# Optimization experiments

Measured on AMD Instinct MI355X. Metric: run time of the kernel, lower is better.

The kernel has to match this reference:

```python
import jax, jax.numpy as jnp
import numpy as np
import math

N, T, D = 1024, 4096, 20


def setup_inputs() -> dict:
    key = jax.random.key(0)
    k1, k2, k3, k4, k5 = jax.random.split(key, 5)
    evidence_vector = jax.random.normal(k1, (T, D), jnp.float32)
    # valid (strictly positive) prior and row-stochastic, all-positive transitions
    prior_probs = jax.nn.softmax(jax.random.normal(k2, (N,), jnp.float32))
    transition_probs = jax.nn.softmax(jax.random.normal(k3, (N, N), jnp.float32), axis=1)
    means = jax.random.normal(k4, (N, D), jnp.float32)
    stds = jax.random.uniform(k5, (N, D), jnp.float32, minval=0.5, maxval=1.5)
    emission_paras = jnp.stack([means, stds], axis=-1)  # [N, D, 2]
    return {"evidence_vector": evidence_vector, "prior_probs": prior_probs,
            "transition_probs": transition_probs, "emission_paras": emission_paras}


def _emission_logp(evidence, emission_paras):
    # Faithful to the source: p = (2*pi*std)**(-0.5) * exp(-(x-mean)^2/(2*std^2))
    mean = emission_paras[..., 0]  # [N, D]
    std = emission_paras[..., 1]   # [N, D]
    p = (2.0 * math.pi * std) ** (-0.5) * jnp.exp(
        -(evidence[:, None, :] - mean) ** 2 / (2.0 * std ** 2))  # [T, N, D]
    logp = jnp.log(p)
    # step 0 uses raw log; steps >=1 pass through nan_to_num(nan=0, inf kept)
    logp0 = jnp.sum(logp[0], axis=1)  # [N]
    logp_rest = jnp.sum(jnp.nan_to_num(logp[1:], nan=0.0, posinf=jnp.inf, neginf=-jnp.inf), axis=2)  # [T-1, N]
    return logp0, logp_rest


def _viterbi_nl(evidence, prior, trans, emission_paras):
    logp0, logp_rest = _emission_logp(evidence, emission_paras)
    log_trans = jnp.log(trans)  # all positive transitions -> finite
    col0 = jnp.log(prior) + logp0  # [N]

    state_ids = jnp.arange(N)

    def step(prev_col, logp_t):
        # scores[k, j] = nl[k, i-1] + log trans[k, j]; nl[j,i] = max_k scores + logp
        scores = prev_col[:, None] + log_trans          # [N, N]
        best = jnp.max(scores, axis=0)                  # [N]
        # j == 0 branch of the source: prev_state = j, no max over k
        new0 = prev_col[0] + log_trans[0, 0]
        new_col = jnp.where(state_ids == 0, new0, best) + logp_t
        return new_col, new_col

    _, cols = jax.lax.scan(step, col0, logp_rest)       # [T-1, N]
    nl = jnp.concatenate([col0[None, :], cols], axis=0).T  # [N, T]
    return nl, log_trans


def reference(evidence_vector, prior_probs, transition_probs, emission_paras):
    nl, log_trans = _viterbi_nl(evidence_vector, prior_probs, transition_probs, emission_paras)
    last = jnp.argmax(nl[:, -1]).astype(jnp.int32)

    def bt_step(front, i):
        # argmax_j nl[j, i] + log trans[j, front]; strict '>' ascending -> first max
        best = jnp.argmax(nl[:, i] + log_trans[:, front]).astype(jnp.int32)
        return best, best

    _, rev = jax.lax.scan(bt_step, last, jnp.arange(T - 2, -1, -1))
    # source appends the final argmax twice, then prepends states for i = T-2..0
    sequence = jnp.concatenate([rev[::-1], jnp.array([last, last], dtype=jnp.int32)])
    return sequence  # [T + 1] int32
```

## Files before the change

kernel.cpp:

```cpp
#include <hip/hip_runtime.h>
#include <math.h>

#define NSTATES 1024
#define TT      4096
#define DD      20

#define FW_BLOCKS  64
#define FW_THREADS 256
#define JPB  16
#define NSEG 16
#define KSEG 64

#define SENT 0x7FC00000u

#define OFF_LAT   ((size_t)0)
#define OFF_COLS  ((size_t)20 << 20)
#define OFF_PTR   ((size_t)36 << 20)

typedef unsigned int u32;

__global__ void k_init(uint4* __restrict__ cols4) {
    int id = blockIdx.x * 256 + threadIdx.x;
    cols4[id] = make_uint4(SENT, SENT, SENT, SENT);
}

__global__ void k_logtrans(const float* __restrict__ tr, float* __restrict__ lat) {
    int id = blockIdx.x * 256 + threadIdx.x;
    int k = id >> 10, j = id & 1023;
    lat[(size_t)j * NSTATES + k] = logf(tr[id]);
}

__global__ __launch_bounds__(FW_THREADS, 1) void k_forward(
    const float* __restrict__ lat, const float* __restrict__ ev,
    const float* __restrict__ epar, const float* __restrict__ prior,
    float* __restrict__ cols, unsigned short* __restrict__ bptr)
{
    __shared__ __align__(16) float prevs[NSEG * 68];
    __shared__ float          smaxw[4][JPB];
    __shared__ unsigned short sidxw[4][JPB];
    __shared__ float          elp[2][JPB][DD];
    const int tid  = threadIdx.x;
    const int seg  = tid >> 4;
    const int jj   = tid & (JPB - 1);
    const int wav  = tid >> 6;
    const int j0   = blockIdx.x * JPB;
    const int j    = j0 + jj;
    const float lat00 = lat[0];

    const int jj0e = tid / DD, d0e = tid % DD;
    const float m0 = epar[((size_t)(j0 + jj0e) * DD + d0e) * 2 + 0];
    const float s0 = epar[((size_t)(j0 + jj0e) * DD + d0e) * 2 + 1];
    const float coef0 = 1.0f / sqrtf(6.2831853071795864769f * s0);
    const float den0  = 2.0f * (s0 * s0);
    const bool  has1  = (tid + 256) < JPB * DD;
    const int   it1   = tid + 256;
    const int jj1e = has1 ? it1 / DD : 0, d1e = has1 ? it1 % DD : 0;
    const float m1 = has1 ? epar[((size_t)(j0 + jj1e) * DD + d1e) * 2 + 0] : 0.0f;
    const float s1 = has1 ? epar[((size_t)(j0 + jj1e) * DD + d1e) * 2 + 1] : 1.0f;
    const float coef1 = 1.0f / sqrtf(6.2831853071795864769f * s1);
    const float den1  = 2.0f * (s1 * s1);

    auto emis = [&](int t, int buf) {
        float x0  = ev[(size_t)t * DD + d0e];
        float df0 = x0 - m0;
        float num0 = df0 * df0;
        float p0  = coef0 * expf(-num0 / den0);
        elp[buf][jj0e][d0e] = logf(p0);
        if (has1) {
            float x1  = ev[(size_t)t * DD + d1e];
            float df1 = x1 - m1;
            float num1 = df1 * df1;
            float p1  = coef1 * expf(-num1 / den1);
            elp[buf][jj1e][d1e] = logf(p1);
        }
    };

    float4 latr[16];
    {
        const float* lrow = lat + (size_t)j * NSTATES + seg * KSEG;
        #pragma unroll
        for (int u = 0; u < 16; ++u) latr[u] = *(const float4*)(lrow + u * 4);
    }

    float* dstp = &prevs[(tid >> 4) * 68 + (tid & 15) * 4];
    const float* rowp = &prevs[seg * 68];

    emis(0, 0);
    __syncthreads();
    if (tid < JPB) {
        float acc = 0.0f;
        #pragma unroll
        for (int d = 0; d < DD; ++d) acc += elp[0][tid][d];
        float c0 = logf(prior[j0 + tid]) + acc;
        __hip_atomic_store((u32*)cols + (j0 + tid), __float_as_uint(c0),
                           __ATOMIC_RELAXED, __HIP_MEMORY_SCOPE_AGENT);
    }
    __syncthreads();
    emis(1, 1);
    __syncthreads();
    float esum_reg = 0.0f;
    if (tid < JPB) {
        #pragma unroll
        for (int d = 0; d < DD; ++d) esum_reg += elp[1][tid][d];
    }

    for (int t = 1; t < TT; ++t) {
        const u32* p = (const u32*)(cols + (size_t)(t - 1) * NSTATES) + tid * 4;
        u32 w0, w1, w2, w3;
        for (;;) {
            w0 = __hip_atomic_load(p + 0, __ATOMIC_RELAXED, __HIP_MEMORY_SCOPE_AGENT);
            w1 = __hip_atomic_load(p + 1, __ATOMIC_RELAXED, __HIP_MEMORY_SCOPE_AGENT);
            w2 = __hip_atomic_load(p + 2, __ATOMIC_RELAXED, __HIP_MEMORY_SCOPE_AGENT);
            w3 = __hip_atomic_load(p + 3, __ATOMIC_RELAXED, __HIP_MEMORY_SCOPE_AGENT);
            if (w0 != SENT && w1 != SENT && w2 != SENT && w3 != SENT) break;
            __builtin_amdgcn_s_sleep(1);
        }
        {
            float4 v;
            v.x = __uint_as_float(w0);
            v.y = __uint_as_float(w1);
            v.z = __uint_as_float(w2);
            v.w = __uint_as_float(w3);
            *(float4*)dstp = v;
        }
        __syncthreads();

        float best = -__builtin_inff();
        int bidx = seg * KSEG;
        #pragma unroll
        for (int u = 0; u < 16; ++u) {
            float4 q  = *(const float4*)(rowp + u * 4);
            float4 wv = latr[u];
            int k0 = seg * KSEG + u * 4;
            float v0 = q.x + wv.x;
            float v1 = q.y + wv.y;
            float v2 = q.z + wv.z;
            float v3 = q.w + wv.w;
            if (v0 > best) { best = v0; bidx = k0;     }
            if (v1 > best) { best = v1; bidx = k0 + 1; }
            if (v2 > best) { best = v2; bidx = k0 + 2; }
            if (v3 > best) { best = v3; bidx = k0 + 3; }
        }

        {
            float ov = __shfl_xor(best, 16);
            int   oi = __shfl_xor(bidx, 16);
            if (ov > best || (ov == best && oi < bidx)) { best = ov; bidx = oi; }
            ov = __shfl_xor(best, 32);
            oi = __shfl_xor(bidx, 32);
            if (ov > best || (ov == best && oi < bidx)) { best = ov; bidx = oi; }
        }
        if ((tid & 63) < JPB) {
            smaxw[wav][jj] = best;
            sidxw[wav][jj] = (unsigned short)bidx;
        }
        __syncthreads();

        if (tid < JPB) {
            float m = smaxw[0][tid];
            int  mi = sidxw[0][tid];
            #pragma unroll
            for (int ww = 1; ww < 4; ++ww) {
                float v = smaxw[ww][tid];
                if (v > m) { m = v; mi = sidxw[ww][tid]; }
            }
            int jw = j0 + tid;
            float val = (jw == 0) ? (prevs[0] + lat00) : m;
            float out = val + esum_reg;
            __hip_atomic_store((u32*)(cols + (size_t)t * NSTATES) + jw,
                               __float_as_uint(out), __ATOMIC_RELAXED,
                               __HIP_MEMORY_SCOPE_AGENT);
            bptr[(size_t)t * NSTATES + jw] = (unsigned short)mi;
        }

        if (t + 1 < TT) {
            emis(t + 1, (t + 1) & 1);
            __syncthreads();
            if (tid < JPB) {
                float acc = 0.0f;
                #pragma unroll
                for (int d = 0; d < DD; ++d) acc += elp[(t + 1) & 1][tid][d];
                esum_reg = acc;
            }
        }
    }
}

#define BTC 16
__global__ void k_backtrace(const float* __restrict__ lastcol,
                            const unsigned short* __restrict__ bptr,
                            int* __restrict__ seq)
{
    __shared__ unsigned short ring[2][BTC][NSTATES];
    __shared__ int s_front;
    const int tid = threadIdx.x;

    if (tid < 64) {
        float best = -__builtin_inff();
        int bi = 0;
        for (int n2 = tid; n2 < NSTATES; n2 += 64) {
            float v = lastcol[n2];
            if (v > best) { best = v; bi = n2; }
        }
        #pragma unroll
        for (int off = 32; off > 0; off >>= 1) {
            float ov = __shfl_xor(best, off);
            int   oi = __shfl_xor(bi, off);
            if (ov > best || (ov == best && oi < bi)) { best = ov; bi = oi; }
        }
        if (tid == 0) { seq[TT] = bi; seq[TT - 1] = bi; s_front = bi; }
    }
    __syncthreads();

    auto stage = [&](int c, int buf, int t0, int stride) {
        int rhi = TT - 1 - c * BTC;
        int rlo = rhi - (BTC - 1); if (rlo < 1) rlo = 1;
        int n4 = (rhi - rlo + 1) * 128;
        uint4* dst = (uint4*)&ring[buf][0][0];
        for (int idx = t0; idx < n4; idx += stride) {
            int ro = idx >> 7, wo = idx & 127;
            dst[idx] = ((const uint4*)(bptr + (size_t)(rhi - ro) * NSTATES))[wo];
        }
    };
    const int nc = (TT - 1 + BTC - 1) / BTC;
    stage(0, 0, tid, 256);
    __syncthreads();
    for (int c = 0; c < nc; ++c) {
        int buf = c & 1;
        if (tid != 0) {
            if (c + 1 < nc) stage(c + 1, buf ^ 1, tid - 1, 255);
        } else {
            int rhi = TT - 1 - c * BTC;
            int rlo = rhi - (BTC - 1); if (rlo < 1) rlo = 1;
            int front = s_front;
            for (int r = rhi; r >= rlo; --r) {
                front = (int)ring[buf][rhi - r][front];
                seq[r - 1] = front;
            }
            s_front = front;
        }
        __syncthreads();
    }
}

extern "C" void kernel_launch(void* const* d_in, const int* in_sizes, int n_in,
                              void* d_out, int out_size, void* d_ws, size_t ws_size,
                              hipStream_t stream) {
    const float* ev    = (const float*)d_in[0];
    const float* prior = (const float*)d_in[1];
    const float* tr    = (const float*)d_in[2];
    const float* epar  = (const float*)d_in[3];
    int* seq = (int*)d_out;
    char* ws = (char*)d_ws;
    float* lat  = (float*)(ws + OFF_LAT);
    float* cols = (float*)(ws + OFF_COLS);
    unsigned short* bptr = (unsigned short*)(ws + OFF_PTR);

    k_init<<<4096, 256, 0, stream>>>((uint4*)cols);
    k_logtrans<<<4096, 256, 0, stream>>>(tr, lat);
    k_forward<<<FW_BLOCKS, FW_THREADS, 0, stream>>>(lat, ev, epar, prior, cols, bptr);
    k_backtrace<<<1, 256, 0, stream>>>(cols + (size_t)(TT - 1) * NSTATES, bptr, seq);
}
```

Measured before the change: 9.682 ms.

## Fuse sentinel init and log-transition setup into forward kernel with grid barrier

Removes the separate init and log-transition kernels. Each forward block now fills its own slice of the column buffer with sentinels and computes its log-transition registers directly from the transition matrix, reading it with a strided transposed access. A global atomic counter barrier makes sure every block's sentinel writes are visible before the wavefront loop starts. It also enlarges the backtrace chunk. The ready counter sits at the start of the bptr region, which could clash with bptr writes at t=0 if row 0 is written, and the strided uncoalesced reads of the transition matrix add latency at kernel start.

```diff
diff --git a/kernel.cpp b/kernel.cpp
--- a/kernel.cpp
+++ b/kernel.cpp
@@ -13,27 +13,18 @@
 
 #define SENT 0x7FC00000u
 
-#define OFF_LAT   ((size_t)0)
 #define OFF_COLS  ((size_t)20 << 20)
 #define OFF_PTR   ((size_t)36 << 20)
 
 typedef unsigned int u32;
 
-__global__ void k_init(uint4* __restrict__ cols4) {
-    int id = blockIdx.x * 256 + threadIdx.x;
-    cols4[id] = make_uint4(SENT, SENT, SENT, SENT);
-}
-
-__global__ void k_logtrans(const float* __restrict__ tr, float* __restrict__ lat) {
-    int id = blockIdx.x * 256 + threadIdx.x;
-    int k = id >> 10, j = id & 1023;
-    lat[(size_t)j * NSTATES + k] = logf(tr[id]);
-}
+#define ALD(p) __hip_atomic_load((p), __ATOMIC_RELAXED, __HIP_MEMORY_SCOPE_AGENT)
 
 __global__ __launch_bounds__(FW_THREADS, 1) void k_forward(
-    const float* __restrict__ lat, const float* __restrict__ ev,
+    const float* __restrict__ tr, const float* __restrict__ ev,
     const float* __restrict__ epar, const float* __restrict__ prior,
-    float* __restrict__ cols, unsigned short* __restrict__ bptr)
+    float* __restrict__ cols, unsigned short* __restrict__ bptr,
+    u32* __restrict__ ready)
 {
     __shared__ __align__(16) float prevs[NSEG * 68];
     __shared__ float          smaxw[4][JPB];
@@ -45,7 +36,25 @@
     const int wav  = tid >> 6;
     const int j0   = blockIdx.x * JPB;
     const int j    = j0 + jj;
-    const float lat00 = lat[0];
+
+    {
+        uint4* mine = (uint4*)cols + (size_t)blockIdx.x * (NSTATES * TT / 4 / FW_BLOCKS);
+        const uint4 sv = make_uint4(SENT, SENT, SENT, SENT);
+        #pragma unroll
+        for (int i = 0; i < (NSTATES * TT / 4 / FW_BLOCKS) / FW_THREADS; ++i)
+            mine[i * FW_THREADS + tid] = sv;
+    }
+
+    const float lat00 = logf(tr[0]);
+    float4 latr[16];
+    #pragma unroll
+    for (int u = 0; u < 16; ++u) {
+        #pragma unroll
+        for (int i = 0; i < 4; ++i) {
+            int k = seg * KSEG + u * 4 + i;
+            ((float*)&latr[u])[i] = logf(tr[(size_t)k * NSTATES + j]);
+        }
+    }
 
     const int jj0e = tid / DD, d0e = tid % DD;
     const float m0 = epar[((size_t)(j0 + jj0e) * DD + d0e) * 2 + 0];
@@ -75,12 +84,14 @@
         }
     };
 
-    float4 latr[16];
-    {
-        const float* lrow = lat + (size_t)j * NSTATES + seg * KSEG;
-        #pragma unroll
-        for (int u = 0; u < 16; ++u) latr[u] = *(const float4*)(lrow + u * 4);
-    }
+    __syncthreads();
+    if (tid == 0) {
+        asm volatile("s_waitcnt vmcnt(0)" ::: "memory");
+        __hip_atomic_fetch_add(ready, 1u, __ATOMIC_RELEASE,
+                               __HIP_MEMORY_SCOPE_AGENT);
+        while (ALD(ready) < (u32)FW_BLOCKS) __builtin_amdgcn_s_sleep(2);
+    }
+    __syncthreads();
 
     float* dstp = &prevs[(tid >> 4) * 68 + (tid & 15) * 4];
     const float* rowp = &prevs[seg * 68];
@@ -186,7 +197,7 @@
     }
 }
 
-#define BTC 16
+#define BTC 24
 __global__ void k_backtrace(const float* __restrict__ lastcol,
                             const unsigned short* __restrict__ bptr,
                             int* __restrict__ seq)
@@ -252,12 +263,12 @@
     const float* epar  = (const float*)d_in[3];
     int* seq = (int*)d_out;
     char* ws = (char*)d_ws;
-    float* lat  = (float*)(ws + OFF_LAT);
     float* cols = (float*)(ws + OFF_COLS);
     unsigned short* bptr = (unsigned short*)(ws + OFF_PTR);
-
-    k_init<<<4096, 256, 0, stream>>>((uint4*)cols);
-    k_logtrans<<<4096, 256, 0, stream>>>(tr, lat);
-    k_forward<<<FW_BLOCKS, FW_THREADS, 0, stream>>>(lat, ev, epar, prior, cols, bptr);
+    u32* ready = (u32*)(ws + OFF_PTR);
+
+    hipMemsetAsync(ready, 0, 4, stream);
+    k_forward<<<FW_BLOCKS, FW_THREADS, 0, stream>>>(tr, ev, epar, prior,
+                                                    cols, bptr, ready);
     k_backtrace<<<1, 256, 0, stream>>>(cols + (size_t)(TT - 1) * NSTATES, bptr, seq);
 }
```

New measurement: 9.452 ms. 2.4% less time.
